# Performance work log

Measured on AMD Instinct MI355X. Metric: run time of the kernel, lower is better.

## Reference

```python
import jax, jax.numpy as jnp
import numpy as np
from jax import lax


def setup_inputs() -> dict:
    key = jax.random.key(0)
    k1, k2, k3 = jax.random.split(key, 3)
    B, C, H, W = 32, 256, 64, 64
    x = jax.random.normal(k1, (B, C, H, W), dtype=jnp.float32)
    # ECA conv1d: 1 in-ch, 1 out-ch, kernel 5 (derived from C=256), no bias
    conv1d_w = jax.random.normal(k2, (1, 1, 5), dtype=jnp.float32) * 0.3
    # Spatial conv2d: 2 in-ch, 1 out-ch, kernel 7, with bias
    conv2d_w = jax.random.normal(k3, (1, 2, 7, 7), dtype=jnp.float32) * 0.1
    conv2d_b = jnp.zeros((1,), dtype=jnp.float32)
    return {"x": x, "conv1d_w": conv1d_w, "conv2d_w": conv2d_w, "conv2d_b": conv2d_b}


def reference(x, conv1d_w, conv2d_w, conv2d_b):
    # --- ECA channel attention ---
    # global avg pool over H,W -> [B, C]
    y = jnp.mean(x, axis=(2, 3))
    # conv1d across the channel axis (treated as length), 1 feature channel
    y = y[:, None, :]  # [B, 1, C]
    y = lax.conv_general_dilated(
        y, conv1d_w, window_strides=(1,), padding=[(2, 2)],
        dimension_numbers=("NCH", "OIH", "NCH"))
    ch_w = jax.nn.sigmoid(y)[:, 0, :, None, None]  # [B, C, 1, 1]
    eca_out = x * ch_w

    # --- spatial attention ---
    max_pool = jnp.max(x, axis=1, keepdims=True)   # [B,1,H,W]
    avg_pool = jnp.mean(x, axis=1, keepdims=True)  # [B,1,H,W]
    sp_in = jnp.concatenate([max_pool, avg_pool], axis=1)  # [B,2,H,W]
    sp = lax.conv_general_dilated(
        sp_in, conv2d_w, window_strides=(1, 1), padding=[(3, 3), (3, 3)],
        dimension_numbers=("NCHW", "OIHW", "NCHW"))
    sp = jax.nn.sigmoid(sp + conv2d_b[None, :, None, None])  # [B,1,H,W]

    return eca_out + x * sp + x
```

## Files before the change

kernel.cpp:

```cpp
#include <hip/hip_runtime.h>
#include <math.h>

#define BB 32
#define CC 256
#define HH 64
#define WW 64
#define HWSZ (HH * WW)
#define NCHUNK 16

typedef float f32x4 __attribute__((ext_vector_type(4)));

__global__ __launch_bounds__(256, 2) void stats_kernel(
    const float* __restrict__ x, float* __restrict__ chan_part,
    float* __restrict__ pool_max, float* __restrict__ pool_sum) {
  const int b = blockIdx.x >> 4;
  const int chunk = blockIdx.x & 15;
  const int hw0 = chunk << 8;
  const int tid = threadIdx.x;
  const int wave = tid >> 6;
  const int lane = tid & 63;
  const int c_base = wave << 6;

  __shared__ float cs[4][64][68];
  __shared__ float4 lmax[4][64];
  __shared__ float4 lsum[4][64];

  const float4* xp =
      (const float4*)(x + ((size_t)b << 20) + ((size_t)c_base << 12) + hw0) + lane;

  float4 mx = make_float4(-3.4e38f, -3.4e38f, -3.4e38f, -3.4e38f);
  float4 sm = make_float4(0.f, 0.f, 0.f, 0.f);

  for (int g = 0; g < 4; ++g) {
    float s[16];
#pragma unroll
    for (int ci = 0; ci < 16; ++ci) {
      const float4 v = xp[(g * 16 + ci) * (HWSZ / 4)];
      mx.x = fmaxf(mx.x, v.x); mx.y = fmaxf(mx.y, v.y);
      mx.z = fmaxf(mx.z, v.z); mx.w = fmaxf(mx.w, v.w);
      sm.x += v.x; sm.y += v.y; sm.z += v.z; sm.w += v.w;
      s[ci] = (v.x + v.y) + (v.z + v.w);
    }
    float4* dst = (float4*)&cs[wave][lane][g * 16];
    dst[0] = make_float4(s[0],  s[1],  s[2],  s[3]);
    dst[1] = make_float4(s[4],  s[5],  s[6],  s[7]);
    dst[2] = make_float4(s[8],  s[9],  s[10], s[11]);
    dst[3] = make_float4(s[12], s[13], s[14], s[15]);
  }

  lmax[wave][lane] = mx;
  lsum[wave][lane] = sm;

  {
    float t0 = 0.f, t1 = 0.f, t2 = 0.f, t3 = 0.f;
#pragma unroll
    for (int j = 0; j < 64; j += 4) {
      t0 += cs[wave][j + 0][lane];
      t1 += cs[wave][j + 1][lane];
      t2 += cs[wave][j + 2][lane];
      t3 += cs[wave][j + 3][lane];
    }
    chan_part[((size_t)(b * NCHUNK + chunk)) * CC + c_base + lane] =
        (t0 + t1) + (t2 + t3);
  }

  __syncthreads();
  if (tid < 64) {
    const float4 a = lmax[0][tid], b4 = lmax[1][tid];
    const float4 c4 = lmax[2][tid], d4 = lmax[3][tid];
    float4 M;
    M.x = fmaxf(fmaxf(a.x, b4.x), fmaxf(c4.x, d4.x));
    M.y = fmaxf(fmaxf(a.y, b4.y), fmaxf(c4.y, d4.y));
    M.z = fmaxf(fmaxf(a.z, b4.z), fmaxf(c4.z, d4.z));
    M.w = fmaxf(fmaxf(a.w, b4.w), fmaxf(c4.w, d4.w));
    const float4 sa = lsum[0][tid], sb = lsum[1][tid];
    const float4 sc = lsum[2][tid], sd = lsum[3][tid];
    float4 S;
    S.x = (sa.x + sb.x) + (sc.x + sd.x);
    S.y = (sa.y + sb.y) + (sc.y + sd.y);
    S.z = (sa.z + sb.z) + (sc.z + sd.z);
    S.w = (sa.w + sb.w) + (sc.w + sd.w);
    ((float4*)(pool_max + ((size_t)b << 12) + hw0))[tid] = M;
    ((float4*)(pool_sum + ((size_t)b << 12) + hw0))[tid] = S;
  }
}

__global__ __launch_bounds__(256) void attn_kernel(
    const float* __restrict__ chan_part, const float* __restrict__ w5,
    float* __restrict__ ch_w,
    const float* __restrict__ pool_max, const float* __restrict__ pool_sum,
    const float* __restrict__ w2, const float* __restrict__ bias,
    float* __restrict__ sp) {
  if (blockIdx.x < BB) {
    __shared__ float m[CC];
    const int b = blockIdx.x;
    const int c = threadIdx.x;
    float s = 0.0f;
#pragma unroll
    for (int k = 0; k < NCHUNK; ++k)
      s += chan_part[(size_t)(b * NCHUNK + k) * CC + c];
    m[c] = s * (1.0f / HWSZ);
    __syncthreads();

    float acc = 0.0f;
#pragma unroll
    for (int k = 0; k < 5; ++k) {
      int cc = c + k - 2;
      float v = (cc >= 0 && cc < CC) ? m[cc] : 0.0f;
      acc = fmaf(v, w5[k], acc);
    }
    ch_w[b * CC + c] = 1.0f / (1.0f + __expf(-acc));
  } else {
    const int idx = (blockIdx.x - BB) * 256 + threadIdx.x;
    const int b = idx >> 12;
    const int hw = idx & (HWSZ - 1);
    const int h = hw >> 6;
    const int w = hw & 63;

    float acc = bias[0];
#pragma unroll
    for (int kh = 0; kh < 7; ++kh) {
      const int hh = h + kh - 3;
      if (hh < 0 || hh >= HH) continue;
#pragma unroll
      for (int kw = 0; kw < 7; ++kw) {
        const int ww = w + kw - 3;
        if (ww < 0 || ww >= WW) continue;
        const int off = b * HWSZ + hh * WW + ww;
        acc = fmaf(pool_max[off], w2[kh * 7 + kw], acc);
        acc = fmaf(pool_sum[off], w2[49 + kh * 7 + kw] * (1.0f / CC), acc);
      }
    }
    sp[idx] = 1.0f / (1.0f + __expf(-acc));
  }
}

__global__ __launch_bounds__(256) void combine_kernel(
    const float* __restrict__ x, const float* __restrict__ ch_w,
    const float* __restrict__ sp, float* __restrict__ out) {
  const int blk = blockIdx.x;
  const int b = blk >> 10;
  const int c = (blk >> 2) & 255;
  const int hw0 = (blk & 3) << 10;
  const int t4 = threadIdx.x;

  const float cw = 1.0f + ch_w[b * CC + c];
  const size_t plane = ((size_t)b << 20) + ((size_t)c << 12) + hw0;
  const float4 x4 = ((const float4*)(x + plane))[t4];
  const float4 s4 = ((const float4*)(sp + ((size_t)b << 12) + hw0))[t4];

  f32x4 o;
  o.x = x4.x * (cw + s4.x);
  o.y = x4.y * (cw + s4.y);
  o.z = x4.z * (cw + s4.z);
  o.w = x4.w * (cw + s4.w);
  __builtin_nontemporal_store(o, (f32x4*)(out + plane) + t4);
}

extern "C" void kernel_launch(void* const* d_in, const int* in_sizes, int n_in,
                              void* d_out, int out_size, void* d_ws, size_t ws_size,
                              hipStream_t stream) {
  const float* x    = (const float*)d_in[0];
  const float* w1   = (const float*)d_in[1];
  const float* w2   = (const float*)d_in[2];
  const float* bias = (const float*)d_in[3];
  float* out = (float*)d_out;

  float* ws = (float*)d_ws;
  float* chan_part = ws;
  float* ch_w      = ws + 131072;
  float* pool_max  = ws + 139264;
  float* pool_sum  = ws + 270336;
  float* sp        = ws + 401408;

  stats_kernel<<<BB * NCHUNK, 256, 0, stream>>>(x, chan_part, pool_max, pool_sum);
  attn_kernel<<<BB + (BB * HWSZ) / 256, 256, 0, stream>>>(
      chan_part, w1, ch_w, pool_max, pool_sum, w2, bias, sp);
  combine_kernel<<<(BB * CC * HWSZ) / (4 * 256), 256, 0, stream>>>(x, ch_w, sp, out);
}
```

Measured before the change: 260.2 us.

## Split stats over channel halves, use wave shuffles, tile spatial conv in LDS

The stats kernel now launches twice as many blocks, each covering half the channels, and writes partial max and sum pools to separate buffers. Per-channel partial sums are reduced with cross-lane shuffles instead of a large shared-memory transpose, which drops the big LDS array. The attention kernel merges the two partial pools while loading a padded halo tile into shared memory and computes the 7x7 conv from LDS without per-tap bounds checks. The aim is more parallelism and lower LDS use in the bandwidth-bound stats pass, in exchange for extra shuffle instructions and a little more workspace traffic.

```diff
diff --git a/kernel.cpp b/kernel.cpp
--- a/kernel.cpp
+++ b/kernel.cpp
@@ -10,20 +10,19 @@
 
 typedef float f32x4 __attribute__((ext_vector_type(4)));
 
-__global__ __launch_bounds__(256, 2) void stats_kernel(
+__global__ __launch_bounds__(256) void stats_kernel(
     const float* __restrict__ x, float* __restrict__ chan_part,
-    float* __restrict__ pool_max, float* __restrict__ pool_sum) {
-  const int b = blockIdx.x >> 4;
-  const int chunk = blockIdx.x & 15;
+    float* __restrict__ pmax0, float* __restrict__ psum0,
+    float* __restrict__ pmax1, float* __restrict__ psum1) {
+  const int b = blockIdx.x >> 5;
+  const int rem = blockIdx.x & 31;
+  const int chunk = rem >> 1;
+  const int half = rem & 1;
   const int hw0 = chunk << 8;
   const int tid = threadIdx.x;
   const int wave = tid >> 6;
   const int lane = tid & 63;
-  const int c_base = wave << 6;
-
-  __shared__ float cs[4][64][68];
-  __shared__ float4 lmax[4][64];
-  __shared__ float4 lsum[4][64];
+  const int c_base = (half << 7) + (wave << 5);
 
   const float4* xp =
       (const float4*)(x + ((size_t)b << 20) + ((size_t)c_base << 12) + hw0) + lane;
@@ -31,7 +30,7 @@
   float4 mx = make_float4(-3.4e38f, -3.4e38f, -3.4e38f, -3.4e38f);
   float4 sm = make_float4(0.f, 0.f, 0.f, 0.f);
 
-  for (int g = 0; g < 4; ++g) {
+  for (int g = 0; g < 2; ++g) {
     float s[16];
 #pragma unroll
     for (int ci = 0; ci < 16; ++ci) {
@@ -41,29 +40,27 @@
       sm.x += v.x; sm.y += v.y; sm.z += v.z; sm.w += v.w;
       s[ci] = (v.x + v.y) + (v.z + v.w);
     }
-    float4* dst = (float4*)&cs[wave][lane][g * 16];
-    dst[0] = make_float4(s[0],  s[1],  s[2],  s[3]);
-    dst[1] = make_float4(s[4],  s[5],  s[6],  s[7]);
-    dst[2] = make_float4(s[8],  s[9],  s[10], s[11]);
-    dst[3] = make_float4(s[12], s[13], s[14], s[15]);
+#pragma unroll
+    for (int ci = 0; ci < 16; ++ci) {
+      float v = s[ci];
+#pragma unroll
+      for (int off = 32; off > 0; off >>= 1) v += __shfl_xor(v, off, 64);
+      s[ci] = v;
+    }
+    if (lane == 0) {
+      float4* cp = (float4*)(chan_part +
+                             ((size_t)(b * NCHUNK + chunk)) * CC + c_base + g * 16);
+      cp[0] = make_float4(s[0],  s[1],  s[2],  s[3]);
+      cp[1] = make_float4(s[4],  s[5],  s[6],  s[7]);
+      cp[2] = make_float4(s[8],  s[9],  s[10], s[11]);
+      cp[3] = make_float4(s[12], s[13], s[14], s[15]);
+    }
   }
 
+  __shared__ float4 lmax[4][64];
+  __shared__ float4 lsum[4][64];
   lmax[wave][lane] = mx;
   lsum[wave][lane] = sm;
-
-  {
-    float t0 = 0.f, t1 = 0.f, t2 = 0.f, t3 = 0.f;
-#pragma unroll
-    for (int j = 0; j < 64; j += 4) {
-      t0 += cs[wave][j + 0][lane];
-      t1 += cs[wave][j + 1][lane];
-      t2 += cs[wave][j + 2][lane];
-      t3 += cs[wave][j + 3][lane];
-    }
-    chan_part[((size_t)(b * NCHUNK + chunk)) * CC + c_base + lane] =
-        (t0 + t1) + (t2 + t3);
-  }
-
   __syncthreads();
   if (tid < 64) {
     const float4 a = lmax[0][tid], b4 = lmax[1][tid];
@@ -80,15 +77,18 @@
     S.y = (sa.y + sb.y) + (sc.y + sd.y);
     S.z = (sa.z + sb.z) + (sc.z + sd.z);
     S.w = (sa.w + sb.w) + (sc.w + sd.w);
-    ((float4*)(pool_max + ((size_t)b << 12) + hw0))[tid] = M;
-    ((float4*)(pool_sum + ((size_t)b << 12) + hw0))[tid] = S;
+    float* pm = half ? pmax1 : pmax0;
+    float* ps = half ? psum1 : psum0;
+    ((float4*)(pm + ((size_t)b << 12) + hw0))[tid] = M;
+    ((float4*)(ps + ((size_t)b << 12) + hw0))[tid] = S;
   }
 }
 
 __global__ __launch_bounds__(256) void attn_kernel(
     const float* __restrict__ chan_part, const float* __restrict__ w5,
     float* __restrict__ ch_w,
-    const float* __restrict__ pool_max, const float* __restrict__ pool_sum,
+    const float* __restrict__ pmax0, const float* __restrict__ psum0,
+    const float* __restrict__ pmax1, const float* __restrict__ psum1,
     const float* __restrict__ w2, const float* __restrict__ bias,
     float* __restrict__ sp) {
   if (blockIdx.x < BB) {
@@ -111,27 +111,42 @@
     }
     ch_w[b * CC + c] = 1.0f / (1.0f + __expf(-acc));
   } else {
-    const int idx = (blockIdx.x - BB) * 256 + threadIdx.x;
-    const int b = idx >> 12;
-    const int hw = idx & (HWSZ - 1);
-    const int h = hw >> 6;
-    const int w = hw & 63;
+    const int sblk = blockIdx.x - BB;
+    const int b = sblk >> 4;
+    const int chunk = sblk & 15;
+    const int r0 = chunk << 2;
+    const int tid = threadIdx.x;
 
+    __shared__ float tmax[10][72];
+    __shared__ float tsum[10][72];
+    for (int idx = tid; idx < 720; idx += 256) {
+      const int row = idx / 72;
+      const int col = idx - row * 72;
+      const int hh = r0 - 3 + row;
+      const int wcol = col - 3;
+      float vm = 0.0f, vs = 0.0f;
+      if (hh >= 0 && hh < HH && wcol >= 0 && wcol < WW) {
+        const int off = (b << 12) + (hh << 6) + wcol;
+        vm = fmaxf(pmax0[off], pmax1[off]);
+        vs = psum0[off] + psum1[off];
+      }
+      tmax[row][col] = vm;
+      tsum[row][col] = vs;
+    }
+    __syncthreads();
+
+    const int lr = tid >> 6;
+    const int w = tid & 63;
     float acc = bias[0];
 #pragma unroll
     for (int kh = 0; kh < 7; ++kh) {
-      const int hh = h + kh - 3;
-      if (hh < 0 || hh >= HH) continue;
 #pragma unroll
       for (int kw = 0; kw < 7; ++kw) {
-        const int ww = w + kw - 3;
-        if (ww < 0 || ww >= WW) continue;
-        const int off = b * HWSZ + hh * WW + ww;
-        acc = fmaf(pool_max[off], w2[kh * 7 + kw], acc);
-        acc = fmaf(pool_sum[off], w2[49 + kh * 7 + kw] * (1.0f / CC), acc);
+        acc = fmaf(tmax[lr + kh][w + kw], w2[kh * 7 + kw], acc);
+        acc = fmaf(tsum[lr + kh][w + kw], w2[49 + kh * 7 + kw] * (1.0f / CC), acc);
       }
     }
-    sp[idx] = 1.0f / (1.0f + __expf(-acc));
+    sp[(b << 12) + (chunk << 8) + tid] = 1.0f / (1.0f + __expf(-acc));
   }
 }
 
@@ -169,12 +184,15 @@
   float* ws = (float*)d_ws;
   float* chan_part = ws;
   float* ch_w      = ws + 131072;
-  float* pool_max  = ws + 139264;
-  float* pool_sum  = ws + 270336;
-  float* sp        = ws + 401408;
+  float* pmax0     = ws + 139264;
+  float* psum0     = ws + 270336;
+  float* pmax1     = ws + 401408;
+  float* psum1     = ws + 532480;
+  float* sp        = ws + 663552;
 
-  stats_kernel<<<BB * NCHUNK, 256, 0, stream>>>(x, chan_part, pool_max, pool_sum);
-  attn_kernel<<<BB + (BB * HWSZ) / 256, 256, 0, stream>>>(
-      chan_part, w1, ch_w, pool_max, pool_sum, w2, bias, sp);
+  stats_kernel<<<BB * NCHUNK * 2, 256, 0, stream>>>(
+      x, chan_part, pmax0, psum0, pmax1, psum1);
+  attn_kernel<<<BB + BB * NCHUNK, 256, 0, stream>>>(
+      chan_part, w1, ch_w, pmax0, psum0, pmax1, psum1, w2, bias, sp);
   combine_kernel<<<(BB * CC * HWSZ) / (4 * 256), 256, 0, stream>>>(x, ch_w, sp, out);
 }
```

After: 259.7 us. No clear change (-0.2%).
